# Optimization experiments

Hardware: AMD Instinct MI355X
Metric: run time of the kernel (lower is better)

Reference implementation:

```python
import jax, jax.numpy as jnp
import numpy as np

EMBED_DIM = 1024
NUM_HEADS = 16
RANK = 32
HEAD_DIM = EMBED_DIM // NUM_HEADS
SCALE = 1.0 / np.sqrt(RANK).astype(np.float32)


def setup_inputs() -> dict:
    key = jax.random.key(0)
    ks = jax.random.split(key, 9)
    B, S = 2, 2048
    def lin(k, fan_in, fan_out):
        bound = 1.0 / np.sqrt(fan_in)
        return jax.random.uniform(k, (fan_in, fan_out), jnp.float32, -bound, bound)
    return {
        "hidden_states": jax.random.normal(ks[0], (B, S, EMBED_DIM), jnp.float32),
        "Wq": lin(ks[1], EMBED_DIM, RANK * NUM_HEADS),
        "bq": jnp.zeros((RANK * NUM_HEADS,), jnp.float32),
        "Wk": lin(ks[2], EMBED_DIM, RANK * NUM_HEADS),
        "bk": jnp.zeros((RANK * NUM_HEADS,), jnp.float32),
        "Wv": lin(ks[3], EMBED_DIM, EMBED_DIM),
        "bv": jnp.zeros((EMBED_DIM,), jnp.float32),
        "Wo": lin(ks[4], EMBED_DIM, EMBED_DIM),
        "bo": jnp.zeros((EMBED_DIM,), jnp.float32),
    }


def reference(hidden_states, Wq, bq, Wk, bk, Wv, bv, Wo, bo):
    B, S, E = hidden_states.shape
    q = (hidden_states @ Wq + bq).reshape(B, S, NUM_HEADS, RANK)      # [b,i,h,r]
    k = (hidden_states @ Wk + bk).reshape(B, S, NUM_HEADS, RANK)      # [b,j,h,r]
    v = (hidden_states @ Wv + bv).reshape(B, S, NUM_HEADS, HEAD_DIM)  # [b,j,h,d]
    # full [b,i,j,h] score tensor, softmax over j (axis=2), as in the torch code
    scores = jnp.einsum('bihr,bjhr->bijh', q, k) * SCALE
    attn = jax.nn.softmax(scores, axis=2)
    out = jnp.einsum('bijh,bjhd->bihd', attn, v).reshape(B, S, E)
    return out @ Wo + bo
```

## Files before the change

### kernel.cpp

```cpp
#include <hip/hip_runtime.h>

#define EMBED   1024
#define NHEADS  16
#define RANK    32
#define HDIM    64
#define BATCH   2
#define SEQ     2048
#define BSQ     (BATCH * SEQ)
#define CEXP    0.25505998f

typedef __attribute__((ext_vector_type(8))) short bf16x8;
typedef __attribute__((ext_vector_type(4))) float f32x4;

__device__ __forceinline__ float bf2f(unsigned short u) {
    union { unsigned int i; float f; } x; x.i = ((unsigned int)u) << 16;
    return x.f;
}
__device__ __forceinline__ unsigned short f2bf(float f) {
    union { float f; unsigned int i; } x; x.f = f;
    unsigned int r = x.i + 0x7FFFu + ((x.i >> 16) & 1u);
    return (unsigned short)(r >> 16);
}

#define ASYNC16(gp, lp) \
    __builtin_amdgcn_global_load_lds( \
        (const __attribute__((address_space(1))) void*)(gp), \
        (__attribute__((address_space(3))) void*)(lp), 16, 0, 0)

#define VMDRAIN() asm volatile("s_waitcnt vmcnt(0)" ::: "memory")

__global__ __launch_bounds__(256) void prep_all(
    const float* __restrict__ hs,
    const float* __restrict__ Wq, const float* __restrict__ Wk,
    const float* __restrict__ Wv, const float* __restrict__ Wo,
    const float* __restrict__ bq, const float* __restrict__ bk,
    const float* __restrict__ bv,
    unsigned short* __restrict__ hsb, unsigned short* __restrict__ wT_all,
    unsigned short* __restrict__ woT, float* __restrict__ ball)
{
    __shared__ float L[64][65];
    const int blk = blockIdx.x;
    const int t = threadIdx.x;

    if (blk < 2048) {
        const size_t i = ((size_t)blk * 256 + t) * 8;
        float4 v0 = *(const float4*)(hs + i);
        float4 v1 = *(const float4*)(hs + i + 4);
        ushort4 o0, o1;
        o0.x = f2bf(v0.x); o0.y = f2bf(v0.y); o0.z = f2bf(v0.z); o0.w = f2bf(v0.w);
        o1.x = f2bf(v1.x); o1.y = f2bf(v1.y); o1.z = f2bf(v1.z); o1.w = f2bf(v1.w);
        *(ushort4*)(hsb + i) = o0;
        *(ushort4*)(hsb + i + 4) = o1;
        return;
    }
    if (blk < 2816) {
        int idx = blk - 2048;
        int z, bx, by;
        if (idx < 256) { z = idx >> 7; int r2 = idx & 127; bx = r2 & 7; by = r2 >> 3; }
        else { idx -= 256; z = 2 + (idx >> 8); int r2 = idx & 255; bx = r2 & 15; by = r2 >> 4; }
        const int Nw = (z < 2) ? 512 : 1024;
        const float* W = (z == 0) ? Wq : (z == 1) ? Wk : (z == 2) ? Wv : Wo;
        unsigned short* dst = (z == 3) ? woT : (wT_all + (size_t)z * 512 * 1024);

        const int r = t >> 2, c0 = (t & 3) * 16;
        const float* src = W + (size_t)(by * 64 + r) * Nw + bx * 64 + c0;
        #pragma unroll
        for (int u = 0; u < 4; u++)
            *(float4*)&L[r][c0 + 4 * u] = *(const float4*)(src + 4 * u);
        __syncthreads();
        unsigned short* drow = dst + (size_t)(bx * 64 + r) * 1024 + by * 64 + c0;
        #pragma unroll
        for (int u4 = 0; u4 < 4; u4++) {
            ushort4 o;
            o.x = f2bf(L[c0 + 4 * u4 + 0][r]);
            o.y = f2bf(L[c0 + 4 * u4 + 1][r]);
            o.z = f2bf(L[c0 + 4 * u4 + 2][r]);
            o.w = f2bf(L[c0 + 4 * u4 + 3][r]);
            *(ushort4*)(drow + 4 * u4) = o;
        }
        return;
    }
    {
        const int i = (blk - 2816) * 256 + t;
        ball[i] = (i < 512) ? bq[i] : (i < 1024) ? bk[i - 512] : bv[i - 1024];
    }
}

__global__ __launch_bounds__(256) void gemm_qkv(
    const unsigned short* __restrict__ A, const unsigned short* __restrict__ BT,
    const float* __restrict__ bias,
    unsigned short* __restrict__ qH, unsigned short* __restrict__ kH,
    unsigned short* __restrict__ vTout)
{
    __shared__ unsigned short As[2 * 128 * 32];
    __shared__ unsigned short Bs[2 * 128 * 32];
    const int K = 1024;
    const int t = threadIdx.x;
    const int lane = t & 63;
    const int li = lane & 15, la = lane >> 4;
    const int w = t >> 6, wm = w >> 1, wn = w & 1;
    const int row0 = blockIdx.y * 128, col0 = blockIdx.x * 128;

    const int sr = lane >> 2, sc2 = (lane & 3) * 8;
    const unsigned short* ag = A + (size_t)(row0 + sr) * K + sc2;
    const unsigned short* bg = BT + (size_t)(col0 + sr) * K + sc2;

    f32x4 acc[4][4];
    #pragma unroll
    for (int i = 0; i < 4; i++)
        #pragma unroll
        for (int j = 0; j < 4; j++)
            acc[i][j] = (f32x4){0.f, 0.f, 0.f, 0.f};

    for (int k0 = 0; k0 < K; k0 += 64) {
        #pragma unroll
        for (int kh = 0; kh < 2; kh++)
            #pragma unroll
            for (int u = 0; u < 2; u++) {
                const int ro = w * 32 + u * 16;
                ASYNC16(ag + (size_t)ro * K + k0 + kh * 32, &As[kh * 4096 + ro * 32]);
                ASYNC16(bg + (size_t)ro * K + k0 + kh * 32, &Bs[kh * 4096 + ro * 32]);
            }
        __syncthreads();
        #pragma unroll
        for (int kh = 0; kh < 2; kh++) {
            bf16x8 af[4], bfr[4];
            #pragma unroll
            for (int mt = 0; mt < 4; mt++)
                af[mt] = *(const bf16x8*)&As[kh * 4096 + (wm * 64 + mt * 16 + li) * 32 + la * 8];
            #pragma unroll
            for (int nt = 0; nt < 4; nt++)
                bfr[nt] = *(const bf16x8*)&Bs[kh * 4096 + (wn * 64 + nt * 16 + li) * 32 + la * 8];
            #pragma unroll
            for (int mt = 0; mt < 4; mt++)
                #pragma unroll
                for (int nt = 0; nt < 4; nt++)
                    acc[mt][nt] = __builtin_amdgcn_mfma_f32_16x16x32_bf16(af[mt], bfr[nt], acc[mt][nt], 0, 0, 0);
        }
        __syncthreads();
    }

    const int bb = row0 >> 11;
    const int jb = (row0 & 2047) + wm * 64;
    #pragma unroll
    for (int nt = 0; nt < 4; nt++) {
        const int col = col0 + wn * 64 + nt * 16 + li;
        const float bval = bias[col];
        if (col < 1024) {
            const int hh = (col & 511) >> 5;
            const int rr = col & 31;
            unsigned short* base = ((col < 512) ? qH : kH)
                + ((size_t)(bb * 16 + hh) * 2048) * 32 + rr;
            #pragma unroll
            for (int mt = 0; mt < 4; mt++)
                #pragma unroll
                for (int r = 0; r < 4; r++)
                    base[(size_t)(jb + mt * 16 + la * 4 + r) * 32] =
                        f2bf(acc[mt][nt][r] + bval);
        } else {
            const int hd = col - 1024;
            unsigned short* dcol = vTout + ((size_t)(bb * 16 + (hd >> 6)) * 64 + (hd & 63)) * SEQ;
            #pragma unroll
            for (int mt = 0; mt < 4; mt++) {
                const int srow = jb + mt * 16 + la * 4;
                ushort4 o;
                o.x = f2bf(acc[mt][nt][0] + bval);
                o.y = f2bf(acc[mt][nt][1] + bval);
                o.z = f2bf(acc[mt][nt][2] + bval);
                o.w = f2bf(acc[mt][nt][3] + bval);
                *(ushort4*)(dcol + srow) = o;
            }
        }
    }
}

__global__ __launch_bounds__(256) void gemm_out(
    const unsigned short* __restrict__ A, const unsigned short* __restrict__ BT,
    const float* __restrict__ bias, float* __restrict__ C)
{
    __shared__ unsigned short As[2 * 64 * 32];
    __shared__ unsigned short Bs[2 * 128 * 32];
    const int K = 1024;
    const int t = threadIdx.x;
    const int lane = t & 63;
    const int li = lane & 15, la = lane >> 4;
    const int w = t >> 6, wm = w >> 1, wn = w & 1;
    const int row0 = blockIdx.y * 64, col0 = blockIdx.x * 128;

    const int sr = lane >> 2, sc2 = (lane & 3) * 8;
    const unsigned short* ag = A + (size_t)(row0 + sr) * K + sc2;
    const unsigned short* bg = BT + (size_t)(col0 + sr) * K + sc2;

    f32x4 acc[2][4];
    #pragma unroll
    for (int i = 0; i < 2; i++)
        #pragma unroll
        for (int j = 0; j < 4; j++)
            acc[i][j] = (f32x4){0.f, 0.f, 0.f, 0.f};

    for (int k0 = 0; k0 < K; k0 += 64) {
        #pragma unroll
        for (int kh = 0; kh < 2; kh++) {
            ASYNC16(ag + (size_t)(w * 16) * K + k0 + kh * 32, &As[kh * 2048 + (w * 16) * 32]);
            #pragma unroll
            for (int u = 0; u < 2; u++) {
                const int ro = w * 32 + u * 16;
                ASYNC16(bg + (size_t)ro * K + k0 + kh * 32, &Bs[kh * 4096 + ro * 32]);
            }
        }
        __syncthreads();
        #pragma unroll
        for (int kh = 0; kh < 2; kh++) {
            bf16x8 af[2], bfr[4];
            #pragma unroll
            for (int mt = 0; mt < 2; mt++)
                af[mt] = *(const bf16x8*)&As[kh * 2048 + (wm * 32 + mt * 16 + li) * 32 + la * 8];
            #pragma unroll
            for (int nt = 0; nt < 4; nt++)
                bfr[nt] = *(const bf16x8*)&Bs[kh * 4096 + (wn * 64 + nt * 16 + li) * 32 + la * 8];
            #pragma unroll
            for (int mt = 0; mt < 2; mt++)
                #pragma unroll
                for (int nt = 0; nt < 4; nt++)
                    acc[mt][nt] = __builtin_amdgcn_mfma_f32_16x16x32_bf16(af[mt], bfr[nt], acc[mt][nt], 0, 0, 0);
        }
        __syncthreads();
    }

    #pragma unroll
    for (int nt = 0; nt < 4; nt++) {
        const int col = col0 + wn * 64 + nt * 16 + li;
        const float bval = bias[col];
        #pragma unroll
        for (int mt = 0; mt < 2; mt++)
            #pragma unroll
            for (int r = 0; r < 4; r++) {
                const int row = row0 + wm * 32 + mt * 16 + la * 4 + r;
                C[(size_t)row * 1024 + col] = acc[mt][nt][r] + bval;
            }
    }
}

__global__ __launch_bounds__(256) void attn_v11(
    const unsigned short* __restrict__ qH,
    const unsigned short* __restrict__ kH,
    const unsigned short* __restrict__ vT,
    unsigned short* __restrict__ ao)
{
    __shared__ unsigned short kt[2][64 * 32];
    __shared__ unsigned short vt[2][64 * 64];
    __shared__ unsigned short P[64 * 72];

    const int t = threadIdx.x;
    const int lane = t & 63;
    const int li = lane & 15, la = lane >> 4;
    const int w = t >> 6;

    const int bh = blockIdx.x & 31;
    const int itile = blockIdx.x >> 5;
    const int i0 = itile * 64;
    const int b = bh >> 4, h = bh & 15;

    bf16x8 qf;
    {
        const unsigned short* qp = qH + ((size_t)bh * 2048 + i0 + w * 16 + li) * 32 + la * 8;
        ushort4 q0 = *(const ushort4*)qp;
        ushort4 q1 = *(const ushort4*)(qp + 4);
        short u[8];
        u[0] = (short)f2bf(bf2f(q0.x) * CEXP);
        u[1] = (short)f2bf(bf2f(q0.y) * CEXP);
        u[2] = (short)f2bf(bf2f(q0.z) * CEXP);
        u[3] = (short)f2bf(bf2f(q0.w) * CEXP);
        u[4] = (short)f2bf(bf2f(q1.x) * CEXP);
        u[5] = (short)f2bf(bf2f(q1.y) * CEXP);
        u[6] = (short)f2bf(bf2f(q1.z) * CEXP);
        u[7] = (short)f2bf(bf2f(q1.w) * CEXP);
        qf = *(const bf16x8*)u;
    }

    bf16x8 vones;
    #pragma unroll
    for (int u2 = 0; u2 < 8; u2++) vones[u2] = (short)0x3F80;

    const int cK8 = ((lane & 3) ^ ((lane >> 3) & 3)) * 8;
    const unsigned short* kpt = kH + (size_t)bh * 2048 * 32
                               + (size_t)(w * 16 + (lane >> 2)) * 32 + cK8;
    const int rV = lane >> 3;
    const int cV8 = ((lane & 7) ^ rV) * 8;
    const unsigned short* vpt0 = vT + ((size_t)bh * 64 + w * 16 + rV) * SEQ + cV8;
    const unsigned short* vpt1 = vpt0 + (size_t)8 * SEQ;

    const int kcol  = (la ^ ((li >> 1) & 3)) * 8;
    const int vcol0 = ((0 * 4 + la) ^ (li & 7)) * 8;
    const int vcol1 = ((1 * 4 + la) ^ (li & 7)) * 8;

    f32x4 accO[4], accl;
    accl = (f32x4){0.f, 0.f, 0.f, 0.f};
    #pragma unroll
    for (int dt = 0; dt < 4; dt++) accO[dt] = (f32x4){0.f, 0.f, 0.f, 0.f};
    const int prow = w * 16 + li;

    ASYNC16(kpt,  &kt[0][w * 512]);
    ASYNC16(vpt0, &vt[0][w * 1024]);
    ASYNC16(vpt1, &vt[0][w * 1024 + 512]);

    #define ATTN_BODY(BUF, OTHER, JPRE)                                            \
    {                                                                              \
        VMDRAIN();                                                                 \
        __syncthreads();                                                           \
        const int jn = (JPRE) & 2047;                                              \
        ASYNC16(kpt + (size_t)jn * 32, &kt[OTHER][w * 512]);                       \
        ASYNC16(vpt0 + jn, &vt[OTHER][w * 1024]);                                  \
        ASYNC16(vpt1 + jn, &vt[OTHER][w * 1024 + 512]);                            \
        f32x4 sc[4];                                                               \
        _Pragma("unroll")                                                          \
        for (int jt = 0; jt < 4; jt++) {                                           \
            const bf16x8 kf = *(const bf16x8*)&kt[BUF][(jt * 16 + li) * 32 + kcol]; \
            sc[jt] = __builtin_amdgcn_mfma_f32_16x16x32_bf16(kf, qf, (f32x4){0.f,0.f,0.f,0.f}, 0, 0, 0); \
        }                                                                          \
        _Pragma("unroll")                                                          \
        for (int jt = 0; jt < 4; jt++) {                                           \
            float e0 = __builtin_amdgcn_exp2f(sc[jt][0]);                          \
            float e1 = __builtin_amdgcn_exp2f(sc[jt][1]);                          \
            float e2 = __builtin_amdgcn_exp2f(sc[jt][2]);                          \
            float e3 = __builtin_amdgcn_exp2f(sc[jt][3]);                          \
            uint2 pk;                                                              \
            asm("v_cvt_pk_bf16_f32 %0, %1, %2" : "=v"(pk.x) : "v"(e0), "v"(e1));   \
            asm("v_cvt_pk_bf16_f32 %0, %1, %2" : "=v"(pk.y) : "v"(e2), "v"(e3));   \
            *(uint2*)&P[prow * 72 + jt * 16 + la * 4] = pk;                        \
        }                                                                          \
        _Pragma("unroll")                                                          \
        for (int ks = 0; ks < 2; ks++) {                                           \
            const bf16x8 pf = *(const bf16x8*)&P[prow * 72 + ks * 32 + la * 8];    \
            accl = __builtin_amdgcn_mfma_f32_16x16x32_bf16(pf, vones, accl, 0, 0, 0); \
            const int vcol = ks ? vcol1 : vcol0;                                   \
            _Pragma("unroll")                                                      \
            for (int dt = 0; dt < 4; dt++) {                                       \
                const bf16x8 vf = *(const bf16x8*)&vt[BUF][(dt * 16 + li) * 64 + vcol]; \
                accO[dt] = __builtin_amdgcn_mfma_f32_16x16x32_bf16(pf, vf, accO[dt], 0, 0, 0); \
            }                                                                      \
        }                                                                          \
    }

    for (int j0 = 0; j0 < SEQ; j0 += 128) {
        ATTN_BODY(0, 1, j0 + 64)
        ATTN_BODY(1, 0, j0 + 128)
    }
    #undef ATTN_BODY

    VMDRAIN();
    __syncthreads();

    float linv[4];
    #pragma unroll
    for (int r = 0; r < 4; r++) linv[r] = 1.f / accl[r];
    #pragma unroll
    for (int dt = 0; dt < 4; dt++)
        #pragma unroll
        for (int r = 0; r < 4; r++) {
            const int row = b * SEQ + i0 + w * 16 + la * 4 + r;
            ao[(size_t)row * 1024 + h * 64 + dt * 16 + li] = f2bf(accO[dt][r] * linv[r]);
        }
}

extern "C" void kernel_launch(void* const* d_in, const int* in_sizes, int n_in,
                              void* d_out, int out_size, void* d_ws, size_t ws_size,
                              hipStream_t stream) {
    const float* hs = (const float*)d_in[0];
    const float* Wq = (const float*)d_in[1];
    const float* bq = (const float*)d_in[2];
    const float* Wk = (const float*)d_in[3];
    const float* bk = (const float*)d_in[4];
    const float* Wv = (const float*)d_in[5];
    const float* bv = (const float*)d_in[6];
    const float* Wo = (const float*)d_in[7];
    const float* bo = (const float*)d_in[8];

    char* p = (char*)d_ws;
    unsigned short* hsb = (unsigned short*)(p);
    unsigned short* wT  = (unsigned short*)(p + 8388608u);
    unsigned short* woT = (unsigned short*)(p + 12582912u);
    float*          ball= (float*)(p + 14680064u);
    unsigned short* qHb = (unsigned short*)(p + 14688256u);
    unsigned short* kHb = (unsigned short*)(p + 18882560u);
    unsigned short* vTb = (unsigned short*)(p + 23076864u);
    unsigned short* ao  = (unsigned short*)(p + 31465472u);

    prep_all<<<dim3(2824), 256, 0, stream>>>(hs, Wq, Wk, Wv, Wo, bq, bk, bv,
                                             hsb, wT, woT, ball);

    gemm_qkv<<<dim3(16, 32), 256, 0, stream>>>(hsb, wT, ball, qHb, kHb, vTb);

    attn_v11<<<dim3(1024), 256, 0, stream>>>(qHb, kHb, vTb, ao);

    gemm_out<<<dim3(8, 64), 256, 0, stream>>>(ao, woT, bo, (float*)d_out);
}
```

Measured before the change: 176.4 us.

## Process two query sub-tiles per wave in attention, halving block size

The attention kernel now runs 128 threads (2 waves) per block, and each wave handles 32 query rows as two 16-row sub-tiles instead of one. Each K fragment and V fragment read from LDS is reused across two MFMAs, and the K/V tile loads are split across fewer waves. This cuts LDS read traffic per unit of compute and the share of barrier overhead. In exchange it raises register pressure from the doubled accumulators, and each block has fewer waves to hide latency.

```diff
diff --git a/kernel.cpp b/kernel.cpp
--- a/kernel.cpp
+++ b/kernel.cpp
@@ -241,7 +241,7 @@
     }
 }
 
-__global__ __launch_bounds__(256) void attn_v11(
+__global__ __launch_bounds__(128) void attn_v12(
     const unsigned short* __restrict__ qH,
     const unsigned short* __restrict__ kH,
     const unsigned short* __restrict__ vT,
@@ -261,9 +261,10 @@
     const int i0 = itile * 64;
     const int b = bh >> 4, h = bh & 15;
 
-    bf16x8 qf;
-    {
-        const unsigned short* qp = qH + ((size_t)bh * 2048 + i0 + w * 16 + li) * 32 + la * 8;
+    bf16x8 qf[2];
+    #pragma unroll
+    for (int iq = 0; iq < 2; iq++) {
+        const unsigned short* qp = qH + ((size_t)bh * 2048 + i0 + w * 32 + iq * 16 + li) * 32 + la * 8;
         ushort4 q0 = *(const ushort4*)qp;
         ushort4 q1 = *(const ushort4*)(qp + 4);
         short u[8];
@@ -275,7 +276,7 @@
         u[5] = (short)f2bf(bf2f(q1.y) * CEXP);
         u[6] = (short)f2bf(bf2f(q1.z) * CEXP);
         u[7] = (short)f2bf(bf2f(q1.w) * CEXP);
-        qf = *(const bf16x8*)u;
+        qf[iq] = *(const bf16x8*)u;
     }
 
     bf16x8 vones;
@@ -284,60 +285,85 @@
 
     const int cK8 = ((lane & 3) ^ ((lane >> 3) & 3)) * 8;
     const unsigned short* kpt = kH + (size_t)bh * 2048 * 32
-                               + (size_t)(w * 16 + (lane >> 2)) * 32 + cK8;
+                               + (size_t)(w * 32 + (lane >> 2)) * 32 + cK8;
     const int rV = lane >> 3;
     const int cV8 = ((lane & 7) ^ rV) * 8;
-    const unsigned short* vpt0 = vT + ((size_t)bh * 64 + w * 16 + rV) * SEQ + cV8;
-    const unsigned short* vpt1 = vpt0 + (size_t)8 * SEQ;
+    const unsigned short* vpt = vT + ((size_t)bh * 64 + w * 32 + rV) * SEQ + cV8;
 
     const int kcol  = (la ^ ((li >> 1) & 3)) * 8;
     const int vcol0 = ((0 * 4 + la) ^ (li & 7)) * 8;
     const int vcol1 = ((1 * 4 + la) ^ (li & 7)) * 8;
 
-    f32x4 accO[4], accl;
-    accl = (f32x4){0.f, 0.f, 0.f, 0.f};
-    #pragma unroll
-    for (int dt = 0; dt < 4; dt++) accO[dt] = (f32x4){0.f, 0.f, 0.f, 0.f};
-    const int prow = w * 16 + li;
-
-    ASYNC16(kpt,  &kt[0][w * 512]);
-    ASYNC16(vpt0, &vt[0][w * 1024]);
-    ASYNC16(vpt1, &vt[0][w * 1024 + 512]);
+    f32x4 accO[2][4], accl[2];
+    #pragma unroll
+    for (int iq = 0; iq < 2; iq++) {
+        accl[iq] = (f32x4){0.f, 0.f, 0.f, 0.f};
+        #pragma unroll
+        for (int dt = 0; dt < 4; dt++) accO[iq][dt] = (f32x4){0.f, 0.f, 0.f, 0.f};
+    }
+    const int prow0 = w * 32 + li;
+    const int prow1 = prow0 + 16;
+
+    ASYNC16(kpt,            &kt[0][(w * 32) * 32]);
+    ASYNC16(kpt + 16 * 32,  &kt[0][(w * 32 + 16) * 32]);
+    #pragma unroll
+    for (int q = 0; q < 4; q++)
+        ASYNC16(vpt + (size_t)q * 8 * SEQ, &vt[0][(w * 32 + q * 8) * 64]);
 
     #define ATTN_BODY(BUF, OTHER, JPRE)                                            \
     {                                                                              \
         VMDRAIN();                                                                 \
         __syncthreads();                                                           \
         const int jn = (JPRE) & 2047;                                              \
-        ASYNC16(kpt + (size_t)jn * 32, &kt[OTHER][w * 512]);                       \
-        ASYNC16(vpt0 + jn, &vt[OTHER][w * 1024]);                                  \
-        ASYNC16(vpt1 + jn, &vt[OTHER][w * 1024 + 512]);                            \
-        f32x4 sc[4];                                                               \
+        ASYNC16(kpt + (size_t)jn * 32,           &kt[OTHER][(w * 32) * 32]);       \
+        ASYNC16(kpt + (size_t)jn * 32 + 16 * 32, &kt[OTHER][(w * 32 + 16) * 32]);  \
+        _Pragma("unroll")                                                          \
+        for (int q = 0; q < 4; q++)                                                \
+            ASYNC16(vpt + jn + (size_t)q * 8 * SEQ, &vt[OTHER][(w * 32 + q * 8) * 64]); \
+        bf16x8 kf[4];                                                              \
+        _Pragma("unroll")                                                          \
+        for (int jt = 0; jt < 4; jt++)                                             \
+            kf[jt] = *(const bf16x8*)&kt[BUF][(jt * 16 + li) * 32 + kcol];         \
+        f32x4 sc0[4], sc1[4];                                                      \
         _Pragma("unroll")                                                          \
         for (int jt = 0; jt < 4; jt++) {                                           \
-            const bf16x8 kf = *(const bf16x8*)&kt[BUF][(jt * 16 + li) * 32 + kcol]; \
-            sc[jt] = __builtin_amdgcn_mfma_f32_16x16x32_bf16(kf, qf, (f32x4){0.f,0.f,0.f,0.f}, 0, 0, 0); \
+            sc0[jt] = __builtin_amdgcn_mfma_f32_16x16x32_bf16(kf[jt], qf[0], (f32x4){0.f,0.f,0.f,0.f}, 0, 0, 0); \
+            sc1[jt] = __builtin_amdgcn_mfma_f32_16x16x32_bf16(kf[jt], qf[1], (f32x4){0.f,0.f,0.f,0.f}, 0, 0, 0); \
         }                                                                          \
         _Pragma("unroll")                                                          \
         for (int jt = 0; jt < 4; jt++) {                                           \
-            float e0 = __builtin_amdgcn_exp2f(sc[jt][0]);                          \
-            float e1 = __builtin_amdgcn_exp2f(sc[jt][1]);                          \
-            float e2 = __builtin_amdgcn_exp2f(sc[jt][2]);                          \
-            float e3 = __builtin_amdgcn_exp2f(sc[jt][3]);                          \
+            float e0 = __builtin_amdgcn_exp2f(sc0[jt][0]);                         \
+            float e1 = __builtin_amdgcn_exp2f(sc0[jt][1]);                         \
+            float e2 = __builtin_amdgcn_exp2f(sc0[jt][2]);                         \
+            float e3 = __builtin_amdgcn_exp2f(sc0[jt][3]);                         \
             uint2 pk;                                                              \
             asm("v_cvt_pk_bf16_f32 %0, %1, %2" : "=v"(pk.x) : "v"(e0), "v"(e1));   \
             asm("v_cvt_pk_bf16_f32 %0, %1, %2" : "=v"(pk.y) : "v"(e2), "v"(e3));   \
-            *(uint2*)&P[prow * 72 + jt * 16 + la * 4] = pk;                        \
+            *(uint2*)&P[prow0 * 72 + jt * 16 + la * 4] = pk;                       \
         }                                                                          \
         _Pragma("unroll")                                                          \
+        for (int jt = 0; jt < 4; jt++) {                                           \
+            float e0 = __builtin_amdgcn_exp2f(sc1[jt][0]);                         \
+            float e1 = __builtin_amdgcn_exp2f(sc1[jt][1]);                         \
+            float e2 = __builtin_amdgcn_exp2f(sc1[jt][2]);                         \
+            float e3 = __builtin_amdgcn_exp2f(sc1[jt][3]);                         \
+            uint2 pk;                                                              \
+            asm("v_cvt_pk_bf16_f32 %0, %1, %2" : "=v"(pk.x) : "v"(e0), "v"(e1));   \
+            asm("v_cvt_pk_bf16_f32 %0, %1, %2" : "=v"(pk.y) : "v"(e2), "v"(e3));   \
+            *(uint2*)&P[prow1 * 72 + jt * 16 + la * 4] = pk;                       \
+        }                                                                          \
+        _Pragma("unroll")                                                          \
         for (int ks = 0; ks < 2; ks++) {                                           \
-            const bf16x8 pf = *(const bf16x8*)&P[prow * 72 + ks * 32 + la * 8];    \
-            accl = __builtin_amdgcn_mfma_f32_16x16x32_bf16(pf, vones, accl, 0, 0, 0); \
+            const bf16x8 pf0 = *(const bf16x8*)&P[prow0 * 72 + ks * 32 + la * 8];  \
+            const bf16x8 pf1 = *(const bf16x8*)&P[prow1 * 72 + ks * 32 + la * 8];  \
+            accl[0] = __builtin_amdgcn_mfma_f32_16x16x32_bf16(pf0, vones, accl[0], 0, 0, 0); \
+            accl[1] = __builtin_amdgcn_mfma_f32_16x16x32_bf16(pf1, vones, accl[1], 0, 0, 0); \
             const int vcol = ks ? vcol1 : vcol0;                                   \
             _Pragma("unroll")                                                      \
             for (int dt = 0; dt < 4; dt++) {                                       \
                 const bf16x8 vf = *(const bf16x8*)&vt[BUF][(dt * 16 + li) * 64 + vcol]; \
-                accO[dt] = __builtin_amdgcn_mfma_f32_16x16x32_bf16(pf, vf, accO[dt], 0, 0, 0); \
+                accO[0][dt] = __builtin_amdgcn_mfma_f32_16x16x32_bf16(pf0, vf, accO[0][dt], 0, 0, 0); \
+                accO[1][dt] = __builtin_amdgcn_mfma_f32_16x16x32_bf16(pf1, vf, accO[1][dt], 0, 0, 0); \
             }                                                                      \
         }                                                                          \
     }
@@ -351,16 +377,19 @@
     VMDRAIN();
     __syncthreads();
 
-    float linv[4];
-    #pragma unroll
-    for (int r = 0; r < 4; r++) linv[r] = 1.f / accl[r];
-    #pragma unroll
-    for (int dt = 0; dt < 4; dt++)
-        #pragma unroll
-        for (int r = 0; r < 4; r++) {
-            const int row = b * SEQ + i0 + w * 16 + la * 4 + r;
-            ao[(size_t)row * 1024 + h * 64 + dt * 16 + li] = f2bf(accO[dt][r] * linv[r]);
-        }
+    #pragma unroll
+    for (int iq = 0; iq < 2; iq++) {
+        float linv[4];
+        #pragma unroll
+        for (int r = 0; r < 4; r++) linv[r] = 1.f / accl[iq][r];
+        #pragma unroll
+        for (int dt = 0; dt < 4; dt++)
+            #pragma unroll
+            for (int r = 0; r < 4; r++) {
+                const int row = b * SEQ + i0 + w * 32 + iq * 16 + la * 4 + r;
+                ao[(size_t)row * 1024 + h * 64 + dt * 16 + li] = f2bf(accO[iq][dt][r] * linv[r]);
+            }
+    }
 }
 
 extern "C" void kernel_launch(void* const* d_in, const int* in_sizes, int n_in,
@@ -391,7 +420,7 @@
 
     gemm_qkv<<<dim3(16, 32), 256, 0, stream>>>(hsb, wT, ball, qHb, kHb, vTb);
 
-    attn_v11<<<dim3(1024), 256, 0, stream>>>(qHb, kHb, vTb, ao);
+    attn_v12<<<dim3(1024), 128, 0, stream>>>(qHb, kHb, vTb, ao);
 
     gemm_out<<<dim3(8, 64), 256, 0, stream>>>(ao, woT, bo, (float*)d_out);
 }
```

New measurement: 178.6 us. No clear change (+1.2%).
